# Kernel optimization log

Hardware: AMD Instinct MI355X
Metric: run time of the kernel (lower is better)

## Reference

```python
import jax, jax.numpy as jnp
import numpy as np

N = 1_000_000      # number of samples
C = 100            # number of classes
N_BINS = 20        # adaptive-ECE bins (equal-count)
TEMPERATURE = 1.0


def setup_inputs() -> dict:
    key = jax.random.key(0)
    k1, k2 = jax.random.split(key)
    logits = jax.random.normal(k1, (N, C), dtype=jnp.float32)
    labels = jax.random.randint(k2, (N,), 0, C)
    return {"logits": logits, "labels": labels}


def reference(logits, labels):
    # softmax with temperature, top-1 confidence + prediction
    softmaxes = jax.nn.softmax(logits / TEMPERATURE, axis=1)
    confidences = jnp.max(softmaxes, axis=1)            # [N]
    predictions = jnp.argmax(softmaxes, axis=1)         # [N]
    accuracies = (predictions == labels).astype(confidences.dtype)  # [N]

    # sort by confidence ascending; carry accuracies along
    order = jnp.argsort(confidences)
    conf_sorted = confidences[order]
    acc_sorted = accuracies[order]

    num = logits.shape[0]
    window = num // N_BINS            # samples per adaptive bin
    n_full = num // window            # number of flushed bins (== N_BINS when divisible)
    m = n_full * window

    # equal-count binning == reshape + mean (replaces the per-sample python loop)
    conf_bins = conf_sorted[:m].reshape(n_full, window).mean(axis=1)  # avg conf / bin
    acc_bins = acc_sorted[:m].reshape(n_full, window).mean(axis=1)    # accuracy / bin

    ece = jnp.sum(jnp.abs(conf_bins - acc_bins)) * (window / num)
    return jnp.reshape(ece, (1,)), acc_bins
```

## Files before the change

kernel.cpp:

```cpp
#include <hip/hip_runtime.h>
#include <stdint.h>

typedef uint32_t u32;
typedef uint64_t u64;
typedef uint8_t  u8;

#define KEY_MIN   0x3C000000u
#define SUBSHIFT  10
#define NBUCK     57344
#define CHUNKS    224
#define NBINS     20
#define NB        19

__device__ __forceinline__ u32 bucket_of(u32 key) {
    if (key < KEY_MIN) return 0u;
    u32 b = (key - KEY_MIN) >> SUBSHIFT;
    return b < (u32)NBUCK ? b : (u32)(NBUCK - 1);
}

template<int CTRL>
__device__ __forceinline__ float dppf(float v) {
    int i = __float_as_int(v);
    int r = __builtin_amdgcn_update_dpp(i, i, CTRL, 0xF, 0xF, false);
    return __int_as_float(r);
}

__global__ __launch_bounds__(256) void k1_conf100(
        const float* __restrict__ logits, const int* __restrict__ labels,
        u32* __restrict__ keys, u8* __restrict__ accb, u32* __restrict__ hist,
        int N) {
    int lane = threadIdx.x & 63;
    int wid  = (blockIdx.x * (blockDim.x >> 6)) + (threadIdx.x >> 6);
    int g    = lane >> 4;
    int sub  = lane & 15;
    int r    = wid * 4 + g;
    if (r >= N) return;

    const float4* row4 = (const float4*)(logits + (size_t)r * 100);
    float4 v0 = row4[sub];
    float4 v1;
    bool has2 = sub < 9;
    if (has2) v1 = row4[sub + 16];
    else      v1 = make_float4(-3.4e38f, -3.4e38f, -3.4e38f, -3.4e38f);

    float m = fmaxf(fmaxf(fmaxf(v0.x, v0.y), fmaxf(v0.z, v0.w)),
                    fmaxf(fmaxf(v1.x, v1.y), fmaxf(v1.z, v1.w)));

    m = fmaxf(m, dppf<0x128>(m));
    m = fmaxf(m, dppf<0x124>(m));
    m = fmaxf(m, dppf<0x122>(m));
    m = fmaxf(m, dppf<0x121>(m));

    int lbl = labels[r];
    bool inHi = lbl >= 64;
    int owner = inHi ? ((lbl - 64) >> 2) : (lbl >> 2);
    int comp  = lbl & 3;
    float4 vv = inHi ? v1 : v0;
    float cand = (comp == 0) ? vv.x : (comp == 1) ? vv.y : (comp == 2) ? vv.z : vv.w;
    bool eq = (sub == owner) && (cand == m);
    unsigned long long bal = __ballot(eq);

    float s = __expf(v0.x - m) + __expf(v0.y - m) + __expf(v0.z - m) + __expf(v0.w - m);
    if (has2) s += __expf(v1.x - m) + __expf(v1.y - m) + __expf(v1.z - m) + __expf(v1.w - m);

    s += dppf<0x128>(s);
    s += dppf<0x124>(s);
    s += dppf<0x122>(s);
    s += dppf<0x121>(s);

    if (sub == 0) {
        float conf = 1.0f / s;
        u32 key = __float_as_uint(conf);
        keys[r] = key;
        accb[r] = ((bal >> (g * 16)) & 0xFFFFull) ? (u8)1 : (u8)0;
        atomicAdd(&hist[bucket_of(key)], 1u);
    }
}

__global__ __launch_bounds__(256) void k1_generic(
        const float* __restrict__ logits, const int* __restrict__ labels,
        u32* __restrict__ keys, u8* __restrict__ accb, u32* __restrict__ hist,
        int N, int C) {
    int i = blockIdx.x * blockDim.x + threadIdx.x;
    if (i >= N) return;
    const float* row = logits + (size_t)i * (size_t)C;
    float m = -3.4e38f, s = 0.f;
    int am = 0;
    for (int c = 0; c < C; c++) {
        float v = row[c];
        float nm = fmaxf(m, v); am = (v > m) ? c : am;
        s = s * __expf(m - nm) + __expf(v - nm); m = nm;
    }
    float conf = 1.0f / s;
    u32 key = __float_as_uint(conf);
    keys[i] = key;
    accb[i] = (labels[i] == am) ? (u8)1 : (u8)0;
    atomicAdd(&hist[bucket_of(key)], 1u);
}

__global__ __launch_bounds__(256) void k2a_sums(
        const u32* __restrict__ hist, u32* __restrict__ partial) {
    int t = threadIdx.x, b = blockIdx.x;
    u32 v = hist[b * 256 + t];
    #pragma unroll
    for (int off = 32; off >= 1; off >>= 1) v += __shfl_xor(v, off);
    __shared__ u32 ws[4];
    if ((t & 63) == 0) ws[t >> 6] = v;
    __syncthreads();
    if (t == 0) partial[b] = ws[0] + ws[1] + ws[2] + ws[3];
}

__global__ __launch_bounds__(256) void k2b_locate(
        const u32* __restrict__ hist, const u32* __restrict__ partial,
        u32* __restrict__ meta, u32 W) {
    __shared__ u32 excl[CHUNKS + 1];
    int t = threadIdx.x;
    int lane = t & 63, w = t >> 6;
    if (w == 0) {
        u32 carry = 0;
        for (int q = 0; q < CHUNKS; q += 64) {
            u32 v = (q + lane < CHUNKS) ? partial[q + lane] : 0u;
            u32 inc = v;
            #pragma unroll
            for (int d = 1; d < 64; d <<= 1) {
                u32 x = __shfl_up(inc, d);
                if (lane >= d) inc += x;
            }
            if (q + lane < CHUNKS) excl[q + lane] = carry + inc - v;
            carry += __shfl(inc, 63);
        }
        if (lane == 0) excl[CHUNKS] = carry;
    }
    __syncthreads();
    for (int j = w; j < NB; j += 4) {
        u32 r = (u32)(j + 1) * W;
        int lo = 0, hi = CHUNKS - 1;
        while (lo < hi) {
            int mid = (lo + hi) >> 1;
            if (excl[mid + 1] < r) lo = mid + 1; else hi = mid;
        }
        int c = lo;
        u32 cum = excl[c];
        for (int q = 0; q < 256; q += 64) {
            u32 v = hist[c * 256 + q + lane];
            u32 inc = v;
            #pragma unroll
            for (int d = 1; d < 64; d <<= 1) {
                u32 x = __shfl_up(inc, d);
                if (lane >= d) inc += x;
            }
            u32 myExcl = cum + inc - v;
            if (v && myExcl < r && r <= myExcl + v) {
                meta[j] = (u32)(c * 256 + q + lane);
                meta[NB + j] = r - myExcl;
            }
            cum += __shfl(inc, 63);
        }
    }
}

__global__ __launch_bounds__(256) void k3_subhist(
        const u32* __restrict__ keys, const u32* __restrict__ meta,
        u32* __restrict__ subhist, int N) {
    __shared__ u32 sB[NB];
    if (threadIdx.x < NB) sB[threadIdx.x] = meta[threadIdx.x];
    __syncthreads();
    int total4 = N >> 2;
    const uint4* k4 = (const uint4*)keys;
    for (int i = blockIdx.x * blockDim.x + threadIdx.x; i < total4;
         i += gridDim.x * blockDim.x) {
        uint4 kv = k4[i];
        u32 ks[4] = {kv.x, kv.y, kv.z, kv.w};
        #pragma unroll
        for (int e = 0; e < 4; e++) {
            u32 b = bucket_of(ks[e]);
            #pragma unroll
            for (int j = 0; j < NB; j++)
                if (b == sB[j]) atomicAdd(&subhist[j * 1024 + (ks[e] & 1023u)], 1u);
        }
    }
    for (int i = (total4 << 2) + blockIdx.x * blockDim.x + threadIdx.x; i < N;
         i += gridDim.x * blockDim.x) {
        u32 k = keys[i];
        u32 b = bucket_of(k);
        for (int j = 0; j < NB; j++)
            if (b == sB[j]) atomicAdd(&subhist[j * 1024 + (k & 1023u)], 1u);
    }
}

__global__ void k4_resolve(const u32* __restrict__ subhist, u32* __restrict__ meta) {
    int j = blockIdx.x;
    int t = threadIdx.x;
    __shared__ u32 sh[256];
    u32 v[4];
    #pragma unroll
    for (int k = 0; k < 4; k++) v[k] = subhist[j * 1024 + t * 4 + k];
    u32 tsum = v[0] + v[1] + v[2] + v[3];
    sh[t] = tsum; __syncthreads();
    for (int d = 1; d < 256; d <<= 1) {
        u32 x = (t >= d) ? sh[t - d] : 0u;
        __syncthreads(); sh[t] += x; __syncthreads();
    }
    u32 run = sh[t] - tsum;
    u32 off = meta[NB + j];
    u32 bkt = meta[j];
    #pragma unroll
    for (int k = 0; k < 4; k++) {
        if (run < off && off <= run + v[k])
            meta[2 * NB + j] = KEY_MIN + (bkt << SUBSHIFT) + (u32)(t * 4 + k);
        run += v[k];
    }
}

__global__ __launch_bounds__(256) void k7_accum(
        const u32* __restrict__ keys, const u8* __restrict__ accb,
        const u32* __restrict__ meta, u64* __restrict__ confQ,
        u32* __restrict__ accCnt, int N) {
    __shared__ unsigned long long lc[4][NBINS];
    __shared__ u32 la[4][NBINS];
    __shared__ u32 sK[NB];
    int t = threadIdx.x;
    int w = t >> 6;
    if (t < 4 * NBINS) { lc[t / NBINS][t % NBINS] = 0ull; la[t / NBINS][t % NBINS] = 0u; }
    if (t < NB) sK[t] = meta[2 * NB + t];
    __syncthreads();
    int total4 = N >> 2;
    const uint4*  k4 = (const uint4*)keys;
    const uchar4* a4 = (const uchar4*)accb;
    for (int i = blockIdx.x * blockDim.x + t; i < total4; i += gridDim.x * blockDim.x) {
        uint4  kv = k4[i];
        uchar4 av = a4[i];
        u32 ks[4] = {kv.x, kv.y, kv.z, kv.w};
        u32 as[4] = {av.x, av.y, av.z, av.w};
        #pragma unroll
        for (int e = 0; e < 4; e++) {
            int bin = 0;
            #pragma unroll
            for (int j = 0; j < NB; j++) bin += (ks[e] > sK[j]) ? 1 : 0;
            u64 q = (u64)(__uint_as_float(ks[e]) * 4294967296.0f);
            atomicAdd(&lc[w][bin], (unsigned long long)q);
            atomicAdd(&la[w][bin], as[e]);
        }
    }
    for (int i = (total4 << 2) + blockIdx.x * blockDim.x + t; i < N;
         i += gridDim.x * blockDim.x) {
        u32 k = keys[i];
        int bin = 0;
        for (int j = 0; j < NB; j++) bin += (k > sK[j]) ? 1 : 0;
        u64 q = (u64)(__uint_as_float(k) * 4294967296.0f);
        atomicAdd(&lc[w][bin], (unsigned long long)q);
        atomicAdd(&la[w][bin], (u32)accb[i]);
    }
    __syncthreads();
    if (t < NBINS) {
        unsigned long long cq = lc[0][t] + lc[1][t] + lc[2][t] + lc[3][t];
        u32 ac = la[0][t] + la[1][t] + la[2][t] + la[3][t];
        if (cq) atomicAdd((unsigned long long*)&confQ[t], cq);
        if (ac) atomicAdd(&accCnt[t], ac);
    }
}

__global__ void k8_final(const u64* __restrict__ confQ, const u32* __restrict__ accCnt,
                         float* __restrict__ out, int W, int N) {
    if (threadIdx.x == 0 && blockIdx.x == 0) {
        double ece = 0.0;
        for (int b = 0; b < NBINS; b++) {
            double cm = (double)confQ[b] * (1.0 / 4294967296.0) / (double)W;
            double am = (double)accCnt[b] / (double)W;
            ece += fabs(cm - am);
            out[1 + b] = (float)am;
        }
        out[0] = (float)(ece * (double)W / (double)N);
    }
}

extern "C" void kernel_launch(void* const* d_in, const int* in_sizes, int n_in,
                              void* d_out, int out_size, void* d_ws, size_t ws_size,
                              hipStream_t stream) {
    const float* logits = (const float*)d_in[0];
    const int*   labels = (const int*)d_in[1];
    int N = in_sizes[1];
    int C = in_sizes[0] / N;
    float* out = (float*)d_out;

    u8* ws = (u8*)d_ws;
    u32* keys = (u32*)ws;
    u8*  accb = ws + (size_t)4 * N;
    size_t aux = ((size_t)5 * N + 255) & ~(size_t)255;
    u64* confQ   = (u64*)(ws + aux);
    u32* accCnt  = (u32*)(ws + aux + 160);
    u32* hist    = (u32*)(ws + aux + 256);
    u32* subhist = (u32*)(ws + aux + 229632);
    u32* meta    = (u32*)(ws + aux + 307456);
    size_t zbytes = 307456 + 228;
    size_t poff = (aux + zbytes + 255) & ~(size_t)255;
    u32* partial = (u32*)(ws + poff);

    hipMemsetAsync(ws + aux, 0, zbytes, stream);

    u32 W = (u32)(N / NBINS);

    if (C == 100) {
        int blocks1 = (N + 15) / 16;
        k1_conf100<<<blocks1, 256, 0, stream>>>(logits, labels, keys, accb, hist, N);
    } else {
        int blocks1 = (N + 255) / 256;
        k1_generic<<<blocks1, 256, 0, stream>>>(logits, labels, keys, accb, hist, N, C);
    }
    k2a_sums  <<<CHUNKS, 256, 0, stream>>>(hist, partial);
    k2b_locate<<<1, 256, 0, stream>>>(hist, partial, meta, W);
    k3_subhist<<<1024, 256, 0, stream>>>(keys, meta, subhist, N);
    k4_resolve<<<NB, 256, 0, stream>>>(subhist, meta);
    k7_accum  <<<1024, 256, 0, stream>>>(keys, accb, meta, confQ, accCnt, N);
    k8_final  <<<1, 64, 0, stream>>>(confQ, accCnt, out, (int)W, N);
}
```

Measured before the change: 157.7 us.

## Stage logits rows through shared memory with coalesced float4 loads

The C=100 confidence kernel now has each block cooperatively load 64 contiguous rows into LDS with fully coalesced float4 loads, then each 16-lane group processes four rows from shared memory. The old per-row loads were strided, with 100-float rows and lanes 9-15 idle on the second load. The block count drops fourfold. This adds 25.6KB of LDS per block and a barrier, which lowers occupancy, and adds a serial loop of four rows per group.

```diff
diff --git a/kernel.cpp b/kernel.cpp
--- a/kernel.cpp
+++ b/kernel.cpp
@@ -29,51 +29,69 @@
         const float* __restrict__ logits, const int* __restrict__ labels,
         u32* __restrict__ keys, u8* __restrict__ accb, u32* __restrict__ hist,
         int N) {
-    int lane = threadIdx.x & 63;
-    int wid  = (blockIdx.x * (blockDim.x >> 6)) + (threadIdx.x >> 6);
+    __shared__ float4 smem[1600];
+    int tid  = threadIdx.x;
+    int lane = tid & 63;
     int g    = lane >> 4;
     int sub  = lane & 15;
-    int r    = wid * 4 + g;
-    if (r >= N) return;
-
-    const float4* row4 = (const float4*)(logits + (size_t)r * 100);
-    float4 v0 = row4[sub];
-    float4 v1;
+    int grp  = (tid >> 6) * 4 + g;
+    int blk  = blockIdx.x;
+    long rowBase = (long)blk * 64;
+
+    const float4* src = (const float4*)(logits + rowBase * 100);
+    long f4total = ((long)N * 100) >> 2;
+    long fbase = rowBase * 25;
+    #pragma unroll
+    for (int s = 0; s < 6; s++) {
+        int idx = s * 256 + tid;
+        if (fbase + idx < f4total) smem[idx] = src[idx];
+    }
+    if (tid < 64) {
+        int idx = 1536 + tid;
+        if (fbase + idx < f4total) smem[idx] = src[idx];
+    }
+    __syncthreads();
+
     bool has2 = sub < 9;
-    if (has2) v1 = row4[sub + 16];
-    else      v1 = make_float4(-3.4e38f, -3.4e38f, -3.4e38f, -3.4e38f);
-
-    float m = fmaxf(fmaxf(fmaxf(v0.x, v0.y), fmaxf(v0.z, v0.w)),
-                    fmaxf(fmaxf(v1.x, v1.y), fmaxf(v1.z, v1.w)));
-
-    m = fmaxf(m, dppf<0x128>(m));
-    m = fmaxf(m, dppf<0x124>(m));
-    m = fmaxf(m, dppf<0x122>(m));
-    m = fmaxf(m, dppf<0x121>(m));
-
-    int lbl = labels[r];
-    bool inHi = lbl >= 64;
-    int owner = inHi ? ((lbl - 64) >> 2) : (lbl >> 2);
-    int comp  = lbl & 3;
-    float4 vv = inHi ? v1 : v0;
-    float cand = (comp == 0) ? vv.x : (comp == 1) ? vv.y : (comp == 2) ? vv.z : vv.w;
-    bool eq = (sub == owner) && (cand == m);
-    unsigned long long bal = __ballot(eq);
-
-    float s = __expf(v0.x - m) + __expf(v0.y - m) + __expf(v0.z - m) + __expf(v0.w - m);
-    if (has2) s += __expf(v1.x - m) + __expf(v1.y - m) + __expf(v1.z - m) + __expf(v1.w - m);
-
-    s += dppf<0x128>(s);
-    s += dppf<0x124>(s);
-    s += dppf<0x122>(s);
-    s += dppf<0x121>(s);
-
-    if (sub == 0) {
-        float conf = 1.0f / s;
-        u32 key = __float_as_uint(conf);
-        keys[r] = key;
-        accb[r] = ((bal >> (g * 16)) & 0xFFFFull) ? (u8)1 : (u8)0;
-        atomicAdd(&hist[bucket_of(key)], 1u);
+    const float4 NEG = make_float4(-3.4e38f, -3.4e38f, -3.4e38f, -3.4e38f);
+    #pragma unroll
+    for (int q = 0; q < 4; q++) {
+        int lr = grp * 4 + q;
+        long r = rowBase + lr;
+        if (r >= N) break;
+        float4 v0 = smem[lr * 25 + sub];
+        float4 v1 = has2 ? smem[lr * 25 + 16 + sub] : NEG;
+
+        float m = fmaxf(fmaxf(fmaxf(v0.x, v0.y), fmaxf(v0.z, v0.w)),
+                        fmaxf(fmaxf(v1.x, v1.y), fmaxf(v1.z, v1.w)));
+        m = fmaxf(m, dppf<0x128>(m));
+        m = fmaxf(m, dppf<0x124>(m));
+        m = fmaxf(m, dppf<0x122>(m));
+        m = fmaxf(m, dppf<0x121>(m));
+
+        int lbl = labels[r];
+        bool inHi = lbl >= 64;
+        int owner = inHi ? ((lbl - 64) >> 2) : (lbl >> 2);
+        int comp  = lbl & 3;
+        float4 vv = inHi ? v1 : v0;
+        float cand = (comp == 0) ? vv.x : (comp == 1) ? vv.y : (comp == 2) ? vv.z : vv.w;
+        bool eq = (sub == owner) && (cand == m);
+        unsigned long long bal = __ballot(eq);
+
+        float s = __expf(v0.x - m) + __expf(v0.y - m) + __expf(v0.z - m) + __expf(v0.w - m);
+        if (has2) s += __expf(v1.x - m) + __expf(v1.y - m) + __expf(v1.z - m) + __expf(v1.w - m);
+        s += dppf<0x128>(s);
+        s += dppf<0x124>(s);
+        s += dppf<0x122>(s);
+        s += dppf<0x121>(s);
+
+        if (sub == 0) {
+            float conf = 1.0f / s;
+            u32 key = __float_as_uint(conf);
+            keys[r] = key;
+            accb[r] = ((bal >> (g * 16)) & 0xFFFFull) ? (u8)1 : (u8)0;
+            atomicAdd(&hist[bucket_of(key)], 1u);
+        }
     }
 }
 
@@ -301,7 +319,7 @@
     u32 W = (u32)(N / NBINS);
 
     if (C == 100) {
-        int blocks1 = (N + 15) / 16;
+        int blocks1 = (N + 63) / 64;
         k1_conf100<<<blocks1, 256, 0, stream>>>(logits, labels, keys, accb, hist, N);
     } else {
         int blocks1 = (N + 255) / 256;
```

Result: slower. 174.6 us (+10.7%).
